# Kernel tuning notes

Measured on AMD Instinct MI355X. Metric: run time of the kernel, lower is better.

Reference implementation:

```python
import jax, jax.numpy as jnp
import numpy as np

N, INPUT_DIM, HIDDEN_DIM, REL_DIM, OUT_DIM = 512, 128, 256, 128, 64


def setup_inputs() -> dict:
    key = jax.random.key(0)
    ks = jax.random.split(key, 9)
    s = lambda fan_in: 1.0 / np.sqrt(fan_in)
    return {
        "node_feats": jax.random.normal(ks[0], (N, INPUT_DIM), dtype=jnp.float32),
        "W1": jax.random.uniform(ks[1], (2 * INPUT_DIM, HIDDEN_DIM), minval=-s(2 * INPUT_DIM), maxval=s(2 * INPUT_DIM), dtype=jnp.float32),
        "b1": jax.random.uniform(ks[2], (HIDDEN_DIM,), minval=-s(2 * INPUT_DIM), maxval=s(2 * INPUT_DIM), dtype=jnp.float32),
        "W2": jax.random.uniform(ks[3], (HIDDEN_DIM, REL_DIM), minval=-s(HIDDEN_DIM), maxval=s(HIDDEN_DIM), dtype=jnp.float32),
        "b2": jax.random.uniform(ks[4], (REL_DIM,), minval=-s(HIDDEN_DIM), maxval=s(HIDDEN_DIM), dtype=jnp.float32),
        "W3": jax.random.uniform(ks[5], (REL_DIM, 64), minval=-s(REL_DIM), maxval=s(REL_DIM), dtype=jnp.float32),
        "b3": jax.random.uniform(ks[6], (64,), minval=-s(REL_DIM), maxval=s(REL_DIM), dtype=jnp.float32),
        "W4": jax.random.uniform(ks[7], (64, OUT_DIM), minval=-s(64), maxval=s(64), dtype=jnp.float32),
        "b4": jax.random.uniform(ks[8], (OUT_DIM,), minval=-s(64), maxval=s(64), dtype=jnp.float32),
    }


def reference(node_feats, W1, b1, W2, b2, W3, b3, W4, b4):
    n, d = node_feats.shape
    # Pairwise concat: pair[i, j] = [node_feats[i], node_feats[j]]  -> [N*N, 2d]
    left = jnp.broadcast_to(node_feats[:, None, :], (n, n, d))
    right = jnp.broadcast_to(node_feats[None, :, :], (n, n, d))
    pairs = jnp.concatenate([left, right], axis=-1).reshape(n * n, 2 * d)
    h = jax.nn.relu(pairs @ W1 + b1)            # [N^2, hidden]
    r = jax.nn.relu(h @ W2 + b2)                # [N^2, rel]
    R = jnp.mean(r, axis=0)                     # [rel]
    out = jax.nn.relu(R @ W3 + b3) @ W4 + b4    # [out_dim]
    return out
```

## Files before the change

kernel.cpp:

```cpp
#include <hip/hip_runtime.h>
#include <hip/hip_fp16.h>

#define NN   512
#define D    128
#define HID  256
#define REL  128
#define ODIM 64

typedef __attribute__((ext_vector_type(4)))  float        f32x4;
typedef __attribute__((ext_vector_type(16))) float        f32x16;
typedef __attribute__((ext_vector_type(8)))  _Float16     f16x8;
typedef __attribute__((ext_vector_type(4)))  unsigned int u32x4;

union H8 { u32x4 u4; f16x8 h8; };

#define WAIT_VM(N) asm volatile("s_waitcnt vmcnt(" #N ")" ::: "memory")

__device__ __forceinline__ void cp16(void* l, const void* g) {
    __builtin_amdgcn_global_load_lds((const __attribute__((address_space(1))) unsigned int*)g,
                                     (__attribute__((address_space(3))) unsigned int*)l, 16, 0, 0);
}

__global__ void kAW(const float* __restrict__ X, const float* __restrict__ W1,
                    const float* __restrict__ b1, _Float16* __restrict__ Aph,
                    _Float16* __restrict__ Bg,
                    const float* __restrict__ W2, _Float16* __restrict__ W2g) {
    int t = threadIdx.x;
    if (blockIdx.x >= 128) {
        int gid = (blockIdx.x - 128) * 256 + t;
        int f = gid >> 6, l = gid & 63;
        int cg = f >> 4, ks = f & 15;
        H8 pkd;
#pragma unroll
        for (int e = 0; e < 8; ++e) {
            int k = ks * 16 + (l >> 5) * 8 + e;
            int c = cg * 32 + (l & 31);
            pkd.h8[e] = (_Float16)W2[k * REL + c];
        }
        *(u32x4*)&W2g[(size_t)gid * 8] = pkd.u4;
        return;
    }
    __shared__ float Xs[4][D];
    int r0 = blockIdx.x * 4;
#pragma unroll
    for (int q = 0; q < 2; ++q) {
        int idx = q * 256 + t;
        Xs[idx >> 7][idx & 127] = X[(r0 + (idx >> 7)) * D + (idx & 127)];
    }
    __syncthreads();
    float a[4], b[4];
    float b1c = b1[t];
#pragma unroll
    for (int r = 0; r < 4; ++r) { a[r] = b1c; b[r] = 0.f; }
#pragma unroll 4
    for (int k = 0; k < D; ++k) {
        float wt = W1[k * HID + t];
        float wb = W1[(D + k) * HID + t];
#pragma unroll
        for (int r = 0; r < 4; ++r) {
            a[r] += Xs[r][k] * wt;
            b[r] += Xs[r][k] * wb;
        }
    }
    int ks = t >> 4, hs = (t >> 3) & 1, e = t & 7;
#pragma unroll
    for (int r = 0; r < 4; ++r) {
        int row = r0 + r;
        Aph[row * HID + t] = (_Float16)a[r];
        Bg[(row >> 4) * 4096 + ks * 256 + hs * 128 + (row & 15) * 8 + e] = (_Float16)b[r];
    }
}

__global__ __launch_bounds__(256, 2) void kB(const _Float16* __restrict__ Aph,
                                             const _Float16* __restrict__ Bg,
                                             const _Float16* __restrict__ W2g,
                                             const float* __restrict__ b2,
                                             float* __restrict__ partial) {
    __shared__ __align__(16) char smem[2][4096];
    __shared__ float redsh[4][2][32];

    int t = threadIdx.x, w = t >> 6, l = t & 63;
    int blk = blockIdx.x;
    int ch = blk & 1, tg = blk >> 1;
    int jt = tg & 31, itb = tg >> 5;
    int l31 = l & 31, hs = l >> 5, j = l & 15;

    H8 w2r[2][16];
#pragma unroll
    for (int cgi = 0; cgi < 2; ++cgi)
#pragma unroll
        for (int ks = 0; ks < 16; ++ks)
            w2r[cgi][ks].u4 = *(const u32x4*)&W2g[(size_t)((((ch * 2 + cgi) * 16 + ks) * 64) + l) * 8];

    H8 brow[16];
#pragma unroll
    for (int ks = 0; ks < 16; ++ks)
        brow[ks].u4 = *(const u32x4*)&Bg[(size_t)jt * 4096 + ks * 256 + hs * 128 + j * 8];

    float b2c0 = b2[ch * 64 + l31];
    float b2c1 = b2[ch * 64 + 32 + l31];

    const f16x8 zero8 = (f16x8)(_Float16)0.f;
    float psum0 = 0.f, psum1 = 0.f;

    cp16(&smem[0][w * 1024 + l * 16], &Aph[(itb * 8 + 2 * w + hs) * HID + l31 * 8]);

#pragma unroll 1
    for (int u = 0; u < 8; ++u) {
        int cur = u & 1;
        if (u < 7) {
            int i0n = itb * 8 + (u + 1) * 64;
            cp16(&smem[cur ^ 1][w * 1024 + l * 16], &Aph[(i0n + 2 * w + hs) * HID + l31 * 8]);
            WAIT_VM(1);
        } else {
            WAIT_VM(0);
        }

        const char* abase = &smem[cur][w * 1024 + (l31 >> 4) * 512 + hs * 16];

        f32x16 acc0, acc1;
#pragma unroll
        for (int r = 0; r < 16; ++r) { acc0[r] = 0.f; acc1[r] = 0.f; }

#pragma unroll
        for (int ks = 0; ks < 16; ++ks) {
            H8 a = *(const H8*)(abase + ks * 32);
            f16x8 sum = a.h8 + brow[ks].h8;
            H8 h; h.h8 = __builtin_elementwise_max(sum, zero8);
            acc0 = __builtin_amdgcn_mfma_f32_32x32x16_f16(h.h8, w2r[0][ks].h8, acc0, 0, 0, 0);
            acc1 = __builtin_amdgcn_mfma_f32_32x32x16_f16(h.h8, w2r[1][ks].h8, acc1, 0, 0, 0);
        }

        float s0 = 0.f, s1 = 0.f;
#pragma unroll
        for (int r = 0; r < 16; ++r) {
            s0 += fmaxf(acc0[r] + b2c0, 0.f);
            s1 += fmaxf(acc1[r] + b2c1, 0.f);
        }
        psum0 += s0; psum1 += s1;
    }

    psum0 += __shfl_xor(psum0, 32);
    psum1 += __shfl_xor(psum1, 32);
    if (l < 32) { redsh[w][0][l] = psum0; redsh[w][1][l] = psum1; }
    __syncthreads();
    if (w == 0 && l < 32) {
        float t0 = redsh[0][0][l] + redsh[1][0][l] + redsh[2][0][l] + redsh[3][0][l];
        float t1 = redsh[0][1][l] + redsh[1][1][l] + redsh[2][1][l] + redsh[3][1][l];
        partial[blk * 64 + l]      = t0;
        partial[blk * 64 + 32 + l] = t1;
    }
}

__global__ void kRC(const float* __restrict__ partial,
                    const float* __restrict__ W3, const float* __restrict__ b3,
                    const float* __restrict__ W4, const float* __restrict__ b4,
                    float* __restrict__ out) {
    __shared__ float sh[256];
    __shared__ float Rsh[REL];
    __shared__ float t1[ODIM];
    int t = threadIdx.x;
    int c = t & 127, g = t >> 7;
    int ch = c >> 6, cc = c & 63;
    float s = 0.f;
#pragma unroll 4
    for (int k = g * 128; k < g * 128 + 128; ++k)
        s += partial[(2 * k + ch) * 64 + cc];
    sh[t] = s;
    __syncthreads();
    if (t < 128) Rsh[t] = (sh[t] + sh[t + 128]) * (1.f / 262144.f);
    __syncthreads();
    if (t < ODIM) {
        float s3 = b3[t];
#pragma unroll 8
        for (int k = 0; k < REL; ++k) s3 += Rsh[k] * W3[k * ODIM + t];
        t1[t] = fmaxf(s3, 0.f);
    }
    __syncthreads();
    if (t < ODIM) {
        float s4 = b4[t];
#pragma unroll 8
        for (int k = 0; k < ODIM; ++k) s4 += t1[k] * W4[k * ODIM + t];
        out[t] = s4;
    }
}

extern "C" void kernel_launch(void* const* d_in, const int* in_sizes, int n_in,
                              void* d_out, int out_size, void* d_ws, size_t ws_size,
                              hipStream_t stream) {
    const float* X  = (const float*)d_in[0];
    const float* W1 = (const float*)d_in[1];
    const float* b1 = (const float*)d_in[2];
    const float* W2 = (const float*)d_in[3];
    const float* b2 = (const float*)d_in[4];
    const float* W3 = (const float*)d_in[5];
    const float* b3 = (const float*)d_in[6];
    const float* W4 = (const float*)d_in[7];
    const float* b4 = (const float*)d_in[8];
    float* out = (float*)d_out;

    char* ws = (char*)d_ws;
    _Float16* Aph     = (_Float16*)ws;
    _Float16* Bg      = (_Float16*)(ws + 262144);
    _Float16* W2g     = (_Float16*)(ws + 524288);
    float*    partial = (float*)(ws + 589824);

    kAW<<<144, 256, 0, stream>>>(X, W1, b1, Aph, Bg, W2, W2g);
    kB<<<512, 256, 0, stream>>>(Aph, Bg, W2g, b2, partial);
    kRC<<<1, 256, 0, stream>>>(partial, W3, b3, W4, b4, out);
}
```

Measured before the change: 41.90 us.

## Halve kB grid, give each block more rows and load A directly from global

The pair-MLP kernel now launches 256 blocks instead of 512. Each block covers 128 contiguous i rows over 16 iterations, so the register-resident W2 and B-row fragments are loaded once and reused across twice as much work. The async global-to-LDS double buffer for A is replaced by direct vector global loads into registers, and launch bounds drop to one block per CU to free registers. The final reduction kernel is updated to match the new block-index layout. The cost is lower occupancy, fewer blocks than before, and no explicit prefetch to hide global load latency between iterations.

```diff
diff --git a/kernel.cpp b/kernel.cpp
--- a/kernel.cpp
+++ b/kernel.cpp
@@ -13,13 +13,6 @@
 typedef __attribute__((ext_vector_type(4)))  unsigned int u32x4;
 
 union H8 { u32x4 u4; f16x8 h8; };
-
-#define WAIT_VM(N) asm volatile("s_waitcnt vmcnt(" #N ")" ::: "memory")
-
-__device__ __forceinline__ void cp16(void* l, const void* g) {
-    __builtin_amdgcn_global_load_lds((const __attribute__((address_space(1))) unsigned int*)g,
-                                     (__attribute__((address_space(3))) unsigned int*)l, 16, 0, 0);
-}
 
 __global__ void kAW(const float* __restrict__ X, const float* __restrict__ W1,
                     const float* __restrict__ b1, _Float16* __restrict__ Aph,
@@ -71,19 +64,19 @@
     }
 }
 
-__global__ __launch_bounds__(256, 2) void kB(const _Float16* __restrict__ Aph,
+__global__ __launch_bounds__(256, 1) void kB(const _Float16* __restrict__ Aph,
                                              const _Float16* __restrict__ Bg,
                                              const _Float16* __restrict__ W2g,
                                              const float* __restrict__ b2,
                                              float* __restrict__ partial) {
-    __shared__ __align__(16) char smem[2][4096];
     __shared__ float redsh[4][2][32];
 
     int t = threadIdx.x, w = t >> 6, l = t & 63;
     int blk = blockIdx.x;
-    int ch = blk & 1, tg = blk >> 1;
-    int jt = tg & 31, itb = tg >> 5;
+    int jt = blk & 31, ch = (blk >> 5) & 1, it = blk >> 6;
+    int i_base = it * 128;
     int l31 = l & 31, hs = l >> 5, j = l & 15;
+    int i_off = 2 * w + (l31 >> 4);
 
     H8 w2r[2][16];
 #pragma unroll
@@ -103,20 +96,14 @@
     const f16x8 zero8 = (f16x8)(_Float16)0.f;
     float psum0 = 0.f, psum1 = 0.f;
 
-    cp16(&smem[0][w * 1024 + l * 16], &Aph[(itb * 8 + 2 * w + hs) * HID + l31 * 8]);
-
 #pragma unroll 1
-    for (int u = 0; u < 8; ++u) {
-        int cur = u & 1;
-        if (u < 7) {
-            int i0n = itb * 8 + (u + 1) * 64;
-            cp16(&smem[cur ^ 1][w * 1024 + l * 16], &Aph[(i0n + 2 * w + hs) * HID + l31 * 8]);
-            WAIT_VM(1);
-        } else {
-            WAIT_VM(0);
-        }
-
-        const char* abase = &smem[cur][w * 1024 + (l31 >> 4) * 512 + hs * 16];
+    for (int u = 0; u < 16; ++u) {
+        const _Float16* arow = &Aph[(i_base + u * 8 + i_off) * HID + hs * 8];
+
+        H8 af[16];
+#pragma unroll
+        for (int ks = 0; ks < 16; ++ks)
+            af[ks].u4 = *(const u32x4*)(arow + ks * 16);
 
         f32x16 acc0, acc1;
 #pragma unroll
@@ -124,8 +111,7 @@
 
 #pragma unroll
         for (int ks = 0; ks < 16; ++ks) {
-            H8 a = *(const H8*)(abase + ks * 32);
-            f16x8 sum = a.h8 + brow[ks].h8;
+            f16x8 sum = af[ks].h8 + brow[ks].h8;
             H8 h; h.h8 = __builtin_elementwise_max(sum, zero8);
             acc0 = __builtin_amdgcn_mfma_f32_32x32x16_f16(h.h8, w2r[0][ks].h8, acc0, 0, 0, 0);
             acc1 = __builtin_amdgcn_mfma_f32_32x32x16_f16(h.h8, w2r[1][ks].h8, acc1, 0, 0, 0);
@@ -164,8 +150,11 @@
     int ch = c >> 6, cc = c & 63;
     float s = 0.f;
 #pragma unroll 4
-    for (int k = g * 128; k < g * 128 + 128; ++k)
-        s += partial[(2 * k + ch) * 64 + cc];
+    for (int bi = g * 64; bi < g * 64 + 64; ++bi) {
+        int itb = bi >> 5, jtb = bi & 31;
+        int blk = (itb << 6) | (ch << 5) | jtb;
+        s += partial[blk * 64 + cc];
+    }
     sh[t] = s;
     __syncthreads();
     if (t < 128) Rsh[t] = (sh[t] + sh[t + 128]) * (1.f / 262144.f);
@@ -206,6 +195,6 @@
     float*    partial = (float*)(ws + 589824);
 
     kAW<<<144, 256, 0, stream>>>(X, W1, b1, Aph, Bg, W2, W2g);
-    kB<<<512, 256, 0, stream>>>(Aph, Bg, W2g, b2, partial);
+    kB<<<256, 256, 0, stream>>>(Aph, Bg, W2g, b2, partial);
     kRC<<<1, 256, 0, stream>>>(partial, W3, b3, W4, b4, out);
 }
```

Result: slower. 51.56 us (+23.0%).
